# Kernel tuning notes

Measured on AMD Instinct MI355X. Metric: run time of the kernel, lower is better.

The kernel has to match this reference:

```python
import jax, jax.numpy as jnp
import numpy as np

N = 2097152          # number of sample points
IN_DIM = 32          # hash-encoding features
HID = 64
OUT_DIM = 4

def _xavier(key, fan_out, fan_in):
    limit = np.sqrt(6.0 / (fan_in + fan_out)).astype(np.float32)
    return jax.random.uniform(key, (fan_out, fan_in), jnp.float32, -limit, limit)

def setup_inputs() -> dict:
    key = jax.random.key(0)
    kx, k0, k1, k2 = jax.random.split(key, 4)
    return {
        "x": jax.random.normal(kx, (N, IN_DIM), jnp.float32),
        "W0": _xavier(k0, HID, IN_DIM),
        "b0": jnp.zeros((HID,), jnp.float32),
        "W1": _xavier(k1, HID, HID),
        "b1": jnp.zeros((HID,), jnp.float32),
        "W2": _xavier(k2, OUT_DIM, HID),
        "b2": jnp.zeros((OUT_DIM,), jnp.float32),
    }

def reference(x, W0, b0, W1, b1, W2, b2):
    # Linear(in->64) + ReLU, Linear(64->64) + ReLU, Linear(64->out)
    h = jax.nn.relu(x @ W0.T + b0)
    h = jax.nn.relu(h @ W1.T + b1)
    return h @ W2.T + b2
```

## Files before the change

### kernel.cpp

```cpp
#include <hip/hip_runtime.h>


typedef float f4 __attribute__((ext_vector_type(4)));
typedef __bf16 bf16x8 __attribute__((ext_vector_type(8)));

#define MFMA(a, b, c) __builtin_amdgcn_mfma_f32_16x16x32_bf16(a, b, c, 0, 0, 0)


__device__ __forceinline__ bf16x8 cvt8(f4 a, f4 b) {
  bf16x8 o;
#pragma unroll
  for (int e = 0; e < 4; ++e) {
    o[e]     = (__bf16)a[e];
    o[e + 4] = (__bf16)b[e];
  }
  return o;
}

__device__ __forceinline__ void split8(f4 a, f4 b, bf16x8& hi, bf16x8& lo) {
#pragma unroll
  for (int e = 0; e < 4; ++e) {
    float fa = a[e], fb = b[e];
    __bf16 ha = (__bf16)fa, hb = (__bf16)fb;
    hi[e]     = ha;
    hi[e + 4] = hb;
    lo[e]     = (__bf16)(fa - (float)ha);
    lo[e + 4] = (__bf16)(fb - (float)hb);
  }
}

#define TILES_PER_WAVE 16
#define ROWS_PER_BLOCK (4 * TILES_PER_WAVE * 16)

__global__ __launch_bounds__(256) void fastmlp_kernel(
    const float* __restrict__ x, const float* __restrict__ W0,
    const float* __restrict__ b0, const float* __restrict__ W1,
    const float* __restrict__ b1, const float* __restrict__ W2,
    const float* __restrict__ b2, float* __restrict__ out) {
  __shared__ float hbuf[4][16 * 68];

  const int tid  = threadIdx.x;
  const int lane = tid & 63;
  const int wid  = tid >> 6;
  const int c    = lane & 15;
  const int g    = lane >> 4;
  float* hw      = hbuf[wid];

  const f4* W0v = (const f4*)W0;
  const f4* W1v = (const f4*)W1;
  const f4* W2v = (const f4*)W2;
  const f4* xv  = (const f4*)x;

  bf16x8 w0f[4], w1f[4][2], w2f[2];
  float b0c[4], b1c[4];
#pragma unroll
  for (int t = 0; t < 4; ++t) {
    const int j = 16 * t + c;
    f4 wa = W0v[j * 8 + g];
    f4 wb = W0v[j * 8 + 4 + g];
    w0f[t] = cvt8(wa, wb);
    b0c[t] = b0[j];
    b1c[t] = b1[j];
#pragma unroll
    for (int kk = 0; kk < 2; ++kk) {
      f4 va = W1v[j * 16 + 8 * kk + g];
      f4 vb = W1v[j * 16 + 8 * kk + 4 + g];
      w1f[t][kk] = cvt8(va, vb);
    }
  }
  {
    const int j   = c & 3;
    const float m = (c < 4) ? 1.0f : 0.0f;
#pragma unroll
    for (int kk = 0; kk < 2; ++kk) {
      f4 va = W2v[j * 16 + 8 * kk + g] * m;
      f4 vb = W2v[j * 16 + 8 * kk + 4 + g] * m;
      w2f[kk] = cvt8(va, vb);
    }
  }
  const float bb2 = (c < 4) ? b2[c] : 0.0f;

  const int rowbase0 = blockIdx.x * ROWS_PER_BLOCK + wid * (TILES_PER_WAVE * 16);

  for (int i = 0; i < TILES_PER_WAVE; ++i) {
    const int rb  = rowbase0 + i * 16;
    const int row = rb + c;

    f4 p0 = xv[row * 8 + g];
    f4 p1 = xv[row * 8 + 4 + g];
    bf16x8 axh, axl;
    split8(p0, p1, axh, axl);

    f4 acc0[4] = {{0.f, 0.f, 0.f, 0.f},
                  {0.f, 0.f, 0.f, 0.f},
                  {0.f, 0.f, 0.f, 0.f},
                  {0.f, 0.f, 0.f, 0.f}};
#pragma unroll
    for (int t = 0; t < 4; ++t) {
      acc0[t] = MFMA(axh, w0f[t], acc0[t]);
      acc0[t] = MFMA(axl, w0f[t], acc0[t]);
    }

#pragma unroll
    for (int t = 0; t < 4; ++t)
#pragma unroll
      for (int r = 0; r < 4; ++r) {
        float v = fmaxf(acc0[t][r] + b0c[t], 0.0f);
        hw[(4 * g + r) * 68 + 16 * t + c] = v;
      }

    bf16x8 ah[2], al[2];
#pragma unroll
    for (int kk = 0; kk < 2; ++kk) {
      f4 q0 = *(const f4*)&hw[c * 68 + 32 * kk + 4 * g];
      f4 q1 = *(const f4*)&hw[c * 68 + 32 * kk + 16 + 4 * g];
      split8(q0, q1, ah[kk], al[kk]);
    }
    f4 acc1[4] = {{0.f, 0.f, 0.f, 0.f},
                  {0.f, 0.f, 0.f, 0.f},
                  {0.f, 0.f, 0.f, 0.f},
                  {0.f, 0.f, 0.f, 0.f}};
#pragma unroll
    for (int t = 0; t < 4; ++t)
#pragma unroll
      for (int kk = 0; kk < 2; ++kk) {
        acc1[t] = MFMA(ah[kk], w1f[t][kk], acc1[t]);
        acc1[t] = MFMA(al[kk], w1f[t][kk], acc1[t]);
      }

#pragma unroll
    for (int t = 0; t < 4; ++t)
#pragma unroll
      for (int r = 0; r < 4; ++r) {
        float v = fmaxf(acc1[t][r] + b1c[t], 0.0f);
        hw[(4 * g + r) * 68 + 16 * t + c] = v;
      }

    bf16x8 ch[2], cl[2];
#pragma unroll
    for (int kk = 0; kk < 2; ++kk) {
      f4 q0 = *(const f4*)&hw[c * 68 + 32 * kk + 4 * g];
      f4 q1 = *(const f4*)&hw[c * 68 + 32 * kk + 16 + 4 * g];
      split8(q0, q1, ch[kk], cl[kk]);
    }
    f4 acc2 = {bb2, bb2, bb2, bb2};
#pragma unroll
    for (int kk = 0; kk < 2; ++kk) {
      acc2 = MFMA(ch[kk], w2f[kk], acc2);
      acc2 = MFMA(cl[kk], w2f[kk], acc2);
    }

    const int srcl = (lane & 3) + ((lane >> 4) << 4);
    const int rsel = (lane >> 2) & 3;
    float vsel = 0.0f;
#pragma unroll
    for (int r = 0; r < 4; ++r) {
      float tr = __shfl(acc2[r], srcl, 64);
      vsel = (rsel == r) ? tr : vsel;
    }
    out[rb * 4 + lane] = vsel;
  }
}

extern "C" void kernel_launch(void* const* d_in, const int* in_sizes, int n_in,
                              void* d_out, int out_size, void* d_ws,
                              size_t ws_size, hipStream_t stream) {
  const float* x  = (const float*)d_in[0];
  const float* W0 = (const float*)d_in[1];
  const float* b0 = (const float*)d_in[2];
  const float* W1 = (const float*)d_in[3];
  const float* b1 = (const float*)d_in[4];
  const float* W2 = (const float*)d_in[5];
  const float* b2 = (const float*)d_in[6];
  float* out      = (float*)d_out;

  const int N    = in_sizes[0] / 32;
  const int grid = N / ROWS_PER_BLOCK;

  fastmlp_kernel<<<grid, 256, 0, stream>>>(x, W0, b0, W1, b1, W2, b2, out);
}
```

Baseline: 393.9 us.

## Transpose MFMA operands to keep activations in registers, prefetch next x tile

Swaps the MFMA operand order so each layer's output lands in registers already shaped as the next layer's B operand. This removes the LDS round trip used to transpose hidden activations between layers. Biases are folded into the accumulator initialisation, and the output is written as a vector store from one lane group instead of through shuffles. The next tile's x is software-prefetched one iteration ahead, at the cost of a few extra registers.

```diff
diff --git a/kernel.cpp b/kernel.cpp
--- a/kernel.cpp
+++ b/kernel.cpp
@@ -5,7 +5,6 @@
 typedef __bf16 bf16x8 __attribute__((ext_vector_type(8)));
 
 #define MFMA(a, b, c) __builtin_amdgcn_mfma_f32_16x16x32_bf16(a, b, c, 0, 0, 0)
-
 
 __device__ __forceinline__ bf16x8 cvt8(f4 a, f4 b) {
   bf16x8 o;
@@ -37,128 +36,101 @@
     const float* __restrict__ b0, const float* __restrict__ W1,
     const float* __restrict__ b1, const float* __restrict__ W2,
     const float* __restrict__ b2, float* __restrict__ out) {
-  __shared__ float hbuf[4][16 * 68];
-
   const int tid  = threadIdx.x;
   const int lane = tid & 63;
   const int wid  = tid >> 6;
   const int c    = lane & 15;
   const int g    = lane >> 4;
-  float* hw      = hbuf[wid];
 
   const f4* W0v = (const f4*)W0;
   const f4* W1v = (const f4*)W1;
   const f4* W2v = (const f4*)W2;
   const f4* xv  = (const f4*)x;
+  f4* outv      = (f4*)out;
 
   bf16x8 w0f[4], w1f[4][2], w2f[2];
-  float b0c[4], b1c[4];
+  f4 b0f[4], b1f[4];
 #pragma unroll
   for (int t = 0; t < 4; ++t) {
-    const int j = 16 * t + c;
-    f4 wa = W0v[j * 8 + g];
-    f4 wb = W0v[j * 8 + 4 + g];
-    w0f[t] = cvt8(wa, wb);
-    b0c[t] = b0[j];
-    b1c[t] = b1[j];
+    const int m = 16 * t + c;
+    w0f[t] = cvt8(W0v[m * 8 + g], W0v[m * 8 + 4 + g]);
 #pragma unroll
-    for (int kk = 0; kk < 2; ++kk) {
-      f4 va = W1v[j * 16 + 8 * kk + g];
-      f4 vb = W1v[j * 16 + 8 * kk + 4 + g];
-      w1f[t][kk] = cvt8(va, vb);
-    }
+    for (int kk = 0; kk < 2; ++kk)
+      w1f[t][kk] = cvt8(W1v[m * 16 + 8 * kk + g], W1v[m * 16 + 8 * kk + 4 + g]);
+    b0f[t] = ((const f4*)b0)[4 * t + g];
+    b1f[t] = ((const f4*)b1)[4 * t + g];
   }
   {
     const int j   = c & 3;
     const float m = (c < 4) ? 1.0f : 0.0f;
 #pragma unroll
-    for (int kk = 0; kk < 2; ++kk) {
-      f4 va = W2v[j * 16 + 8 * kk + g] * m;
-      f4 vb = W2v[j * 16 + 8 * kk + 4 + g] * m;
-      w2f[kk] = cvt8(va, vb);
-    }
+    for (int kk = 0; kk < 2; ++kk)
+      w2f[kk] = cvt8(W2v[j * 16 + 8 * kk + g] * m,
+                     W2v[j * 16 + 8 * kk + 4 + g] * m);
   }
-  const float bb2 = (c < 4) ? b2[c] : 0.0f;
+  const f4 b2v  = *(const f4*)b2;
+  const f4 zero = {0.f, 0.f, 0.f, 0.f};
+  const f4 acc2init = (g == 0) ? b2v : zero;
 
   const int rowbase0 = blockIdx.x * ROWS_PER_BLOCK + wid * (TILES_PER_WAVE * 16);
 
+  f4 p0 = xv[(rowbase0 + c) * 8 + g];
+  f4 p1 = xv[(rowbase0 + c) * 8 + 4 + g];
+
+#pragma unroll 1
   for (int i = 0; i < TILES_PER_WAVE; ++i) {
-    const int rb  = rowbase0 + i * 16;
-    const int row = rb + c;
+    const int rb = rowbase0 + i * 16;
+    const f4 cur0 = p0, cur1 = p1;
+    if (i + 1 < TILES_PER_WAVE) {
+      p0 = xv[(rb + 16 + c) * 8 + g];
+      p1 = xv[(rb + 16 + c) * 8 + 4 + g];
+    }
 
-    f4 p0 = xv[row * 8 + g];
-    f4 p1 = xv[row * 8 + 4 + g];
     bf16x8 axh, axl;
-    split8(p0, p1, axh, axl);
-
-    f4 acc0[4] = {{0.f, 0.f, 0.f, 0.f},
-                  {0.f, 0.f, 0.f, 0.f},
-                  {0.f, 0.f, 0.f, 0.f},
-                  {0.f, 0.f, 0.f, 0.f}};
+    split8(cur0, cur1, axh, axl);
+    f4 acc0[4];
 #pragma unroll
     for (int t = 0; t < 4; ++t) {
-      acc0[t] = MFMA(axh, w0f[t], acc0[t]);
-      acc0[t] = MFMA(axl, w0f[t], acc0[t]);
+      acc0[t] = b0f[t];
+      acc0[t] = MFMA(w0f[t], axh, acc0[t]);
+      acc0[t] = MFMA(w0f[t], axl, acc0[t]);
     }
-
+    f4 h0[4];
 #pragma unroll
     for (int t = 0; t < 4; ++t)
 #pragma unroll
-      for (int r = 0; r < 4; ++r) {
-        float v = fmaxf(acc0[t][r] + b0c[t], 0.0f);
-        hw[(4 * g + r) * 68 + 16 * t + c] = v;
+      for (int r = 0; r < 4; ++r) h0[t][r] = fmaxf(acc0[t][r], 0.0f);
+
+    bf16x8 bh[2], bl[2];
+#pragma unroll
+    for (int kk = 0; kk < 2; ++kk) split8(h0[2 * kk], h0[2 * kk + 1], bh[kk], bl[kk]);
+    f4 acc1[4];
+#pragma unroll
+    for (int t = 0; t < 4; ++t) {
+      acc1[t] = b1f[t];
+#pragma unroll
+      for (int kk = 0; kk < 2; ++kk) {
+        acc1[t] = MFMA(w1f[t][kk], bh[kk], acc1[t]);
+        acc1[t] = MFMA(w1f[t][kk], bl[kk], acc1[t]);
       }
-
-    bf16x8 ah[2], al[2];
-#pragma unroll
-    for (int kk = 0; kk < 2; ++kk) {
-      f4 q0 = *(const f4*)&hw[c * 68 + 32 * kk + 4 * g];
-      f4 q1 = *(const f4*)&hw[c * 68 + 32 * kk + 16 + 4 * g];
-      split8(q0, q1, ah[kk], al[kk]);
     }
-    f4 acc1[4] = {{0.f, 0.f, 0.f, 0.f},
-                  {0.f, 0.f, 0.f, 0.f},
-                  {0.f, 0.f, 0.f, 0.f},
-                  {0.f, 0.f, 0.f, 0.f}};
+    f4 h1[4];
 #pragma unroll
     for (int t = 0; t < 4; ++t)
 #pragma unroll
-      for (int kk = 0; kk < 2; ++kk) {
-        acc1[t] = MFMA(ah[kk], w1f[t][kk], acc1[t]);
-        acc1[t] = MFMA(al[kk], w1f[t][kk], acc1[t]);
-      }
-
-#pragma unroll
-    for (int t = 0; t < 4; ++t)
-#pragma unroll
-      for (int r = 0; r < 4; ++r) {
-        float v = fmaxf(acc1[t][r] + b1c[t], 0.0f);
-        hw[(4 * g + r) * 68 + 16 * t + c] = v;
-      }
+      for (int r = 0; r < 4; ++r) h1[t][r] = fmaxf(acc1[t][r], 0.0f);
 
     bf16x8 ch[2], cl[2];
 #pragma unroll
-    for (int kk = 0; kk < 2; ++kk) {
-      f4 q0 = *(const f4*)&hw[c * 68 + 32 * kk + 4 * g];
-      f4 q1 = *(const f4*)&hw[c * 68 + 32 * kk + 16 + 4 * g];
-      split8(q0, q1, ch[kk], cl[kk]);
-    }
-    f4 acc2 = {bb2, bb2, bb2, bb2};
+    for (int kk = 0; kk < 2; ++kk) split8(h1[2 * kk], h1[2 * kk + 1], ch[kk], cl[kk]);
+    f4 acc2 = acc2init;
 #pragma unroll
     for (int kk = 0; kk < 2; ++kk) {
-      acc2 = MFMA(ch[kk], w2f[kk], acc2);
-      acc2 = MFMA(cl[kk], w2f[kk], acc2);
+      acc2 = MFMA(w2f[kk], ch[kk], acc2);
+      acc2 = MFMA(w2f[kk], cl[kk], acc2);
     }
 
-    const int srcl = (lane & 3) + ((lane >> 4) << 4);
-    const int rsel = (lane >> 2) & 3;
-    float vsel = 0.0f;
-#pragma unroll
-    for (int r = 0; r < 4; ++r) {
-      float tr = __shfl(acc2[r], srcl, 64);
-      vsel = (rsel == r) ? tr : vsel;
-    }
-    out[rb * 4 + lane] = vsel;
+    if (g == 0) outv[rb + c] = acc2;
   }
 }
 
```

Result: no change. 389.0 us (-1.3%).
